# Kernel tuning notes

Hardware: AMD Instinct MI355X
Metric: run time of the kernel (lower is better)

Reference implementation:

```python
import jax, jax.numpy as jnp
import numpy as np

B, D, H1, H2, J, Q, O = 32768, 35, 256, 256, 12, 7, 5


def setup_inputs() -> dict:
    key = jax.random.key(0)
    ks = jax.random.split(key, 16)
    s = 0.05
    inp = {
        "x": jax.random.uniform(ks[0], (B, D), dtype=jnp.float32),
        "judge_ids": jax.random.randint(ks[1], (B,), 0, J, dtype=jnp.int32),
        # shared layers
        "W1_w": jax.random.normal(ks[2], (H1, D + 1), jnp.float32) * s,
        "W1_b": jnp.zeros((H1,), jnp.float32),
        "W2_w": jax.random.normal(ks[3], (H2, H1 + 1), jnp.float32) * s,
        "W2_b": jnp.zeros((H2,), jnp.float32),
        # judge-specific layers (stacked over J experts)
        "W1a_w": jax.random.normal(ks[4], (J, H1, D + 1), jnp.float32) * s,
        "W1a_b": jnp.zeros((J, H1), jnp.float32),
        "W2a_w": jax.random.normal(ks[5], (J, H2, H1 + 1), jnp.float32) * s,
        "W2a_b": jnp.zeros((J, H2), jnp.float32),
        # per-question output heads (shared + judge-specific)
        "V_w": jax.random.normal(ks[6], (Q, O, H2 + 1), jnp.float32) * s,
        "V_b": jnp.zeros((Q, O), jnp.float32),
        "Va_w": jax.random.normal(ks[7], (J, Q, O, H2 + 1), jnp.float32) * s,
        "Va_b": jnp.zeros((J, Q, O), jnp.float32),
    }
    return inp


def _append_ones(a):
    return jnp.concatenate([a, jnp.ones((a.shape[0], 1), a.dtype)], axis=1)


def reference(x, judge_ids, W1_w, W1_b, W2_w, W2_b, W1a_w, W1a_b, W2a_w, W2a_b, V_w, V_b, Va_w, Va_b):
    ids = judge_ids.astype(jnp.int32)
    xb = _append_ones(x)                                   # (B, D+1)
    # layer 1: shared + judge-routed
    a1 = jnp.einsum('bi,jhi->bjh', xb, W1a_w)              # (B, J, H1)
    j1 = jnp.take_along_axis(a1, ids[:, None, None], axis=1)[:, 0] + W1a_b[ids]
    z1 = jax.nn.relu(xb @ W1_w.T + W1_b + j1)              # (B, H1)
    z1b = _append_ones(z1)                                 # (B, H1+1)
    # layer 2
    a2 = jnp.einsum('bh,jgh->bjg', z1b, W2a_w)             # (B, J, H2)
    j2 = jnp.take_along_axis(a2, ids[:, None, None], axis=1)[:, 0] + W2a_b[ids]
    z2 = jax.nn.relu(z1b @ W2_w.T + W2_b + j2)             # (B, H2)
    z2b = _append_ones(z2)                                 # (B, H2+1)
    # per-question heads
    shared = jnp.einsum('bh,qoh->bqo', z2b, V_w) + V_b     # (B, Q, O)
    aV = jnp.einsum('bh,jqoh->bjqo', z2b, Va_w)            # (B, J, Q, O)
    jV = jnp.take_along_axis(aV, ids[:, None, None, None], axis=1)[:, 0] + Va_b[ids]
    return jax.nn.softmax(shared + jV, axis=-1)            # (B, Q, O)
```

## Files before the change

kernel.cpp:

```cpp
#include <hip/hip_runtime.h>
#include <stdint.h>

#define B_N   32768
#define D_IN  35
#define NJ    12
#define NQ    7
#define NO    5
#define QO    35
#define TILE  32
#define TPJ   128
#define CAPJ  (TPJ * TILE)
#define MAXT  1040

typedef __bf16  v8bf  __attribute__((ext_vector_type(8)));
typedef float   f32x4 __attribute__((ext_vector_type(4)));

__device__ __forceinline__ unsigned short f2bf(float f) {
    unsigned int u = __builtin_bit_cast(unsigned int, f);
    u += 0x7FFFu + ((u >> 16) & 1u);
    return (unsigned short)(u >> 16);
}
__device__ __forceinline__ unsigned int pack2(float a, float b) {
    return (unsigned int)f2bf(a) | ((unsigned int)f2bf(b) << 16);
}

__global__ void k_prep(const int* __restrict__ ids,
                       const float* __restrict__ W1_w, const float* __restrict__ W1_b,
                       const float* __restrict__ W2_w, const float* __restrict__ W2_b,
                       const float* __restrict__ W1a_w, const float* __restrict__ W1a_b,
                       const float* __restrict__ W2a_w, const float* __restrict__ W2a_b,
                       const float* __restrict__ V_w,  const float* __restrict__ V_b,
                       const float* __restrict__ Va_w, const float* __restrict__ Va_b,
                       unsigned short* __restrict__ w1c, unsigned short* __restrict__ w2c,
                       unsigned short* __restrict__ vc,
                       float* __restrict__ bias1, float* __restrict__ bias2,
                       float* __restrict__ biasv,
                       int* __restrict__ cursor, int* __restrict__ perm)
{
    const int tid = blockIdx.x * blockDim.x + threadIdx.x;
    const int nth = gridDim.x * blockDim.x;

    if (blockIdx.x < B_N / 256) {
        __shared__ int lh[NJ], lb[NJ];
        const int lt = threadIdx.x;
        const int s0 = blockIdx.x * 256;
        if (lt < NJ) lh[lt] = 0;
        __syncthreads();
        int id = ids[s0 + lt];
        int rank = atomicAdd(&lh[id], 1);
        __syncthreads();
        if (lt < NJ)
            lb[lt] = lh[lt] ? atomicAdd(&cursor[lt], lh[lt]) : 0;
        __syncthreads();
        int pos = lb[id] + rank;
        if (pos < CAPJ) perm[id * CAPJ + pos] = s0 + lt;
    }

    for (int q = tid; q < NJ * 256 * 64; q += nth) {
        int k4 = (q & 63) << 2, h = (q >> 6) & 255, jj = q >> 14;
        const float* a = &W2_w[h * 257 + k4];
        const float* b = &W2a_w[(jj * 256 + h) * 257 + k4];
        ushort4 o;
        o.x = f2bf(a[0] + b[0]); o.y = f2bf(a[1] + b[1]);
        o.z = f2bf(a[2] + b[2]); o.w = f2bf(a[3] + b[3]);
        *(ushort4*)&w2c[(size_t)q << 2] = o;
    }
    for (int q = tid; q < NJ * 256 * 16; q += nth) {
        int k4 = (q & 15) << 2, h = (q >> 4) & 255, jj = q >> 12;
        ushort4 o;
        float v[4];
#pragma unroll
        for (int e = 0; e < 4; ++e) {
            int k = k4 + e;
            v[e] = (k < D_IN) ? (W1_w[h * 36 + k] + W1a_w[(jj * 256 + h) * 36 + k]) : 0.f;
        }
        o.x = f2bf(v[0]); o.y = f2bf(v[1]); o.z = f2bf(v[2]); o.w = f2bf(v[3]);
        *(ushort4*)&w1c[(size_t)q << 2] = o;
    }
    for (int q = tid; q < NJ * 48 * 64; q += nth) {
        int k4 = (q & 63) << 2, qo = (q >> 6) % 48, jj = q / (48 * 64);
        ushort4 o;
        if (qo < QO) {
            const float* a = &V_w[qo * 257 + k4];
            const float* b = &Va_w[(jj * QO + qo) * 257 + k4];
            o.x = f2bf(a[0] + b[0]); o.y = f2bf(a[1] + b[1]);
            o.z = f2bf(a[2] + b[2]); o.w = f2bf(a[3] + b[3]);
        } else {
            o.x = o.y = o.z = o.w = 0;
        }
        *(ushort4*)&vc[(size_t)q << 2] = o;
    }
    for (int i = tid; i < NJ * 256; i += nth) {
        int h = i & 255, jj = i >> 8;
        bias1[i] = W1_w[h * 36 + 35] + W1a_w[(jj * 256 + h) * 36 + 35] + W1_b[h] + W1a_b[i];
        bias2[i] = W2_w[h * 257 + 256] + W2a_w[(jj * 256 + h) * 257 + 256] + W2_b[h] + W2a_b[i];
    }
    for (int i = tid; i < NJ * 48; i += nth) {
        int qo = i % 48, jj = i / 48;
        float v = 0.f;
        if (qo < QO) v = V_w[qo * 257 + 256] + Va_w[(jj * QO + qo) * 257 + 256]
                       + V_b[qo] + Va_b[jj * QO + qo];
        biasv[i] = v;
    }
}

__global__ __launch_bounds__(256, 4) void k_main(
    const float* __restrict__ x, float* __restrict__ out,
    const int* __restrict__ perm, const int* __restrict__ counts,
    const unsigned short* __restrict__ w1c, const unsigned short* __restrict__ w2c,
    const unsigned short* __restrict__ vc,
    const float* __restrict__ bias1, const float* __restrict__ bias2,
    const float* __restrict__ biasv)
{
    __shared__ __align__(16) unsigned short s_z1[TILE][264];
    __shared__ __align__(16) union {
        unsigned short xb[TILE][72];
        float          lg[TILE][40];
    } s_u;
    __shared__ int s_rows[TILE];

    const int bid = blockIdx.x;

    int nt = 0;
#pragma unroll
    for (int jj = 0; jj < NJ; ++jj) nt += (counts[jj] + 31) >> 5;
    if (bid >= nt) return;

    const int q8 = nt >> 3, r8 = nt & 7;
    const int xcd = bid & 7, idx = bid >> 3;
    const int lbid = (xcd < r8 ? xcd * (q8 + 1) : r8 * (q8 + 1) + (xcd - r8) * q8) + idx;

    int j = 0, tb_j = 0, cj = 0, pacc = 0;
#pragma unroll
    for (int jj = 0; jj < NJ; ++jj) {
        int c = counts[jj];
        if (lbid >= pacc) { j = jj; tb_j = pacc; cj = c; }
        pacc += (c + 31) >> 5;
    }
    if (cj > CAPJ) cj = CAPJ;
    const int ts = (lbid - tb_j) << 5;

    const int tid  = threadIdx.x;
    const int lane = tid & 63;
    const int wave = tid >> 6;
    const int l16  = lane & 15;
    const int lk   = lane >> 4;

    const unsigned short* w1p = w1c + ((size_t)j << 14) + (size_t)(wave * 64) * 64;
    v8bf w1a0[4], w1a1[4];
#pragma unroll
    for (int t = 0; t < 4; ++t) {
        const unsigned short* rp = w1p + (t * 16 + l16) * 64;
        w1a0[t] = *(const v8bf*)&rp[lk * 8];
        w1a1[t] = *(const v8bf*)&rp[32 + lk * 8];
    }

    if (tid < TILE)
        s_rows[tid] = (ts + tid < cj) ? perm[j * CAPJ + ts + tid] : -1;
    for (int i = tid; i < TILE * 36; i += 256) ((unsigned int*)s_u.xb)[i] = 0u;
    __syncthreads();

    for (int i = tid; i < TILE * D_IN; i += 256) {
        int s = i / D_IN, k = i - s * D_IN;
        int r = s_rows[s];
        s_u.xb[s][k] = f2bf(r >= 0 ? x[(size_t)r * D_IN + k] : 0.f);
    }
    __syncthreads();

    const f32x4 vz = {0.f, 0.f, 0.f, 0.f};

    {
        v8bf b1[2][2];
#pragma unroll
        for (int mt = 0; mt < 2; ++mt) {
            b1[mt][0] = *(const v8bf*)&s_u.xb[mt * 16 + l16][lk * 8];
            b1[mt][1] = *(const v8bf*)&s_u.xb[mt * 16 + l16][32 + lk * 8];
        }
        f32x4 acc[4][2];
#pragma unroll
        for (int t = 0; t < 4; ++t) { acc[t][0] = vz; acc[t][1] = vz; }
        __builtin_amdgcn_s_setprio(1);
#pragma unroll
        for (int t = 0; t < 4; ++t) {
#pragma unroll
            for (int mt = 0; mt < 2; ++mt) {
                acc[t][mt] = __builtin_amdgcn_mfma_f32_16x16x32_bf16(w1a0[t], b1[mt][0], acc[t][mt], 0, 0, 0);
                acc[t][mt] = __builtin_amdgcn_mfma_f32_16x16x32_bf16(w1a1[t], b1[mt][1], acc[t][mt], 0, 0, 0);
            }
        }
        __builtin_amdgcn_s_setprio(0);
        const unsigned short* w2p = w2c + ((size_t)j << 16) + (size_t)(wave * 64) * 256;
        v8bf a2pre[4];
#pragma unroll
        for (int gt = 0; gt < 4; ++gt)
            a2pre[gt] = *(const v8bf*)&w2p[(gt * 16 + l16) * 256 + lk * 8];

#pragma unroll
        for (int t = 0; t < 4; ++t) {
            f32x4 bz = *(const f32x4*)&bias1[j * 256 + wave * 64 + t * 16 + lk * 4];
#pragma unroll
            for (int mt = 0; mt < 2; ++mt) {
                float v0 = acc[t][mt][0] + bz[0], v1 = acc[t][mt][1] + bz[1];
                float v2 = acc[t][mt][2] + bz[2], v3 = acc[t][mt][3] + bz[3];
                v0 = v0 > 0.f ? v0 : 0.f; v1 = v1 > 0.f ? v1 : 0.f;
                v2 = v2 > 0.f ? v2 : 0.f; v3 = v3 > 0.f ? v3 : 0.f;
                uint2 pk; pk.x = pack2(v0, v1); pk.y = pack2(v2, v3);
                *(uint2*)&s_z1[mt * 16 + l16][wave * 64 + t * 16 + lk * 4] = pk;
            }
        }
        __syncthreads();

        f32x4 acc2[4][2];
#pragma unroll
        for (int gt = 0; gt < 4; ++gt) { acc2[gt][0] = vz; acc2[gt][1] = vz; }
        __builtin_amdgcn_s_setprio(1);
        {
            v8bf bb0 = *(const v8bf*)&s_z1[l16][lk * 8];
            v8bf bb1 = *(const v8bf*)&s_z1[16 + l16][lk * 8];
#pragma unroll
            for (int gt = 0; gt < 4; ++gt) {
                acc2[gt][0] = __builtin_amdgcn_mfma_f32_16x16x32_bf16(a2pre[gt], bb0, acc2[gt][0], 0, 0, 0);
                acc2[gt][1] = __builtin_amdgcn_mfma_f32_16x16x32_bf16(a2pre[gt], bb1, acc2[gt][1], 0, 0, 0);
            }
        }
#pragma unroll 2
        for (int hc = 1; hc < 8; ++hc) {
            v8bf bb0 = *(const v8bf*)&s_z1[l16][hc * 32 + lk * 8];
            v8bf bb1 = *(const v8bf*)&s_z1[16 + l16][hc * 32 + lk * 8];
#pragma unroll
            for (int gt = 0; gt < 4; ++gt) {
                v8bf a = *(const v8bf*)&w2p[(gt * 16 + l16) * 256 + hc * 32 + lk * 8];
                acc2[gt][0] = __builtin_amdgcn_mfma_f32_16x16x32_bf16(a, bb0, acc2[gt][0], 0, 0, 0);
                acc2[gt][1] = __builtin_amdgcn_mfma_f32_16x16x32_bf16(a, bb1, acc2[gt][1], 0, 0, 0);
            }
        }
        __builtin_amdgcn_s_setprio(0);
        const unsigned short* vp = vc + (size_t)j * 12288 + (size_t)(wave * 16) * 256;
        v8bf a3pre;
        if (wave < 3) a3pre = *(const v8bf*)&vp[l16 * 256 + lk * 8];

        __syncthreads();
#pragma unroll
        for (int gt = 0; gt < 4; ++gt) {
            f32x4 bz = *(const f32x4*)&bias2[j * 256 + wave * 64 + gt * 16 + lk * 4];
#pragma unroll
            for (int mt = 0; mt < 2; ++mt) {
                float v0 = acc2[gt][mt][0] + bz[0], v1 = acc2[gt][mt][1] + bz[1];
                float v2 = acc2[gt][mt][2] + bz[2], v3 = acc2[gt][mt][3] + bz[3];
                v0 = v0 > 0.f ? v0 : 0.f; v1 = v1 > 0.f ? v1 : 0.f;
                v2 = v2 > 0.f ? v2 : 0.f; v3 = v3 > 0.f ? v3 : 0.f;
                uint2 pk; pk.x = pack2(v0, v1); pk.y = pack2(v2, v3);
                *(uint2*)&s_z1[mt * 16 + l16][wave * 64 + gt * 16 + lk * 4] = pk;
            }
        }
        __syncthreads();

        if (wave < 3) {
            f32x4 av[2] = {vz, vz};
            __builtin_amdgcn_s_setprio(1);
            {
                v8bf bb0 = *(const v8bf*)&s_z1[l16][lk * 8];
                v8bf bb1 = *(const v8bf*)&s_z1[16 + l16][lk * 8];
                av[0] = __builtin_amdgcn_mfma_f32_16x16x32_bf16(a3pre, bb0, av[0], 0, 0, 0);
                av[1] = __builtin_amdgcn_mfma_f32_16x16x32_bf16(a3pre, bb1, av[1], 0, 0, 0);
            }
#pragma unroll 4
            for (int gc = 1; gc < 8; ++gc) {
                v8bf bb0 = *(const v8bf*)&s_z1[l16][gc * 32 + lk * 8];
                v8bf bb1 = *(const v8bf*)&s_z1[16 + l16][gc * 32 + lk * 8];
                v8bf a = *(const v8bf*)&vp[l16 * 256 + gc * 32 + lk * 8];
                av[0] = __builtin_amdgcn_mfma_f32_16x16x32_bf16(a, bb0, av[0], 0, 0, 0);
                av[1] = __builtin_amdgcn_mfma_f32_16x16x32_bf16(a, bb1, av[1], 0, 0, 0);
            }
            __builtin_amdgcn_s_setprio(0);
            int qb = wave * 16 + lk * 4;
            if (qb < 36) {
                f32x4 bz = *(const f32x4*)&biasv[j * 48 + qb];
#pragma unroll
                for (int mt = 0; mt < 2; ++mt) {
                    f32x4 v = av[mt] + bz;
                    *(f32x4*)&s_u.lg[mt * 16 + l16][qb] = v;
                }
            }
        }
    }
    __syncthreads();

    if (tid < TILE * NQ) {
        int s = tid / NQ, qq = tid - s * NQ;
        int r = s_rows[s];
        if (r >= 0) {
            float l[NO], mx = -1e30f;
#pragma unroll
            for (int o = 0; o < NO; ++o) {
                l[o] = s_u.lg[s][qq * NO + o];
                mx = l[o] > mx ? l[o] : mx;
            }
            float sum = 0.f, e[NO];
#pragma unroll
            for (int o = 0; o < NO; ++o) { e[o] = __expf(l[o] - mx); sum += e[o]; }
            float inv = 1.f / sum;
            float* op = out + (size_t)r * QO + qq * NO;
#pragma unroll
            for (int o = 0; o < NO; ++o) op[o] = e[o] * inv;
        }
    }
}

extern "C" void kernel_launch(void* const* d_in, const int* in_sizes, int n_in,
                              void* d_out, int out_size, void* d_ws, size_t ws_size,
                              hipStream_t stream)
{
    const float* x     = (const float*)d_in[0];
    const int*   ids   = (const int*)d_in[1];
    const float* W1_w  = (const float*)d_in[2];
    const float* W1_b  = (const float*)d_in[3];
    const float* W2_w  = (const float*)d_in[4];
    const float* W2_b  = (const float*)d_in[5];
    const float* W1a_w = (const float*)d_in[6];
    const float* W1a_b = (const float*)d_in[7];
    const float* W2a_w = (const float*)d_in[8];
    const float* W2a_b = (const float*)d_in[9];
    const float* V_w   = (const float*)d_in[10];
    const float* V_b   = (const float*)d_in[11];
    const float* Va_w  = (const float*)d_in[12];
    const float* Va_b  = (const float*)d_in[13];
    float* out = (float*)d_out;

    char* ws = (char*)d_ws;
    size_t off = 0;
    auto take = [&](size_t nbytes) -> void* {
        void* p = ws + off;
        off = (off + nbytes + 255) & ~(size_t)255;
        return p;
    };
    unsigned short* w1c = (unsigned short*)take((size_t)NJ * 256 * 64 * 2);
    unsigned short* w2c = (unsigned short*)take((size_t)NJ * 256 * 256 * 2);
    unsigned short* vc  = (unsigned short*)take((size_t)NJ * 48 * 256 * 2);
    float* bias1        = (float*)take((size_t)NJ * 256 * 4);
    float* bias2        = (float*)take((size_t)NJ * 256 * 4);
    float* biasv        = (float*)take((size_t)NJ * 48 * 4);
    int* cursor         = (int*)take(NJ * 4);
    int* perm           = (int*)take((size_t)NJ * CAPJ * 4);

    hipMemsetAsync(cursor, 0, NJ * sizeof(int), stream);
    k_prep<<<768, 256, 0, stream>>>(ids, W1_w, W1_b, W2_w, W2_b, W1a_w, W1a_b,
                                    W2a_w, W2a_b, V_w, V_b, Va_w, Va_b,
                                    w1c, w2c, vc, bias1, bias2, biasv,
                                    cursor, perm);
    k_main<<<MAXT, 256, 0, stream>>>(x, out, perm, cursor,
                                     w1c, w2c, vc, bias1, bias2, biasv);
}
```

Baseline: 47.07 us.

## Pre-sort and bf16-pack x rows per judge in prep kernel

The prep kernel now writes each input row, converted to bf16 and zero-padded to 64 columns, into a judge-sorted buffer at the same slot as its perm entry. The main kernel then loads its layer-1 MFMA operands straight from that contiguous buffer into registers, instead of gathering x through the row indices into shared memory. This removes the LDS zero-fill, the scattered gather, two block barriers and the shared union in the main kernel. In exchange the prep kernel does strided per-thread row reads and 128-byte writes, and tile tail slots read uninitialized padding that only feeds rows that are never stored.

```diff
diff --git a/kernel.cpp b/kernel.cpp
--- a/kernel.cpp
+++ b/kernel.cpp
@@ -24,7 +24,7 @@
     return (unsigned int)f2bf(a) | ((unsigned int)f2bf(b) << 16);
 }
 
-__global__ void k_prep(const int* __restrict__ ids,
+__global__ void k_prep(const int* __restrict__ ids, const float* __restrict__ x,
                        const float* __restrict__ W1_w, const float* __restrict__ W1_b,
                        const float* __restrict__ W2_w, const float* __restrict__ W2_b,
                        const float* __restrict__ W1a_w, const float* __restrict__ W1a_b,
@@ -35,7 +35,8 @@
                        unsigned short* __restrict__ vc,
                        float* __restrict__ bias1, float* __restrict__ bias2,
                        float* __restrict__ biasv,
-                       int* __restrict__ cursor, int* __restrict__ perm)
+                       int* __restrict__ cursor, int* __restrict__ perm,
+                       unsigned short* __restrict__ xsorted)
 {
     const int tid = blockIdx.x * blockDim.x + threadIdx.x;
     const int nth = gridDim.x * blockDim.x;
@@ -53,7 +54,24 @@
             lb[lt] = lh[lt] ? atomicAdd(&cursor[lt], lh[lt]) : 0;
         __syncthreads();
         int pos = lb[id] + rank;
-        if (pos < CAPJ) perm[id * CAPJ + pos] = s0 + lt;
+        if (pos < CAPJ) {
+            perm[id * CAPJ + pos] = s0 + lt;
+            const float* xr = x + (size_t)(s0 + lt) * D_IN;
+            unsigned short* xd = xsorted + ((size_t)id * CAPJ + pos) * 64;
+#pragma unroll
+            for (int c = 0; c < 8; ++c) {
+                uint4 w;
+                w.x = pack2(c * 8 + 0 < D_IN ? xr[c * 8 + 0] : 0.f,
+                            c * 8 + 1 < D_IN ? xr[c * 8 + 1] : 0.f);
+                w.y = pack2(c * 8 + 2 < D_IN ? xr[c * 8 + 2] : 0.f,
+                            c * 8 + 3 < D_IN ? xr[c * 8 + 3] : 0.f);
+                w.z = pack2(c * 8 + 4 < D_IN ? xr[c * 8 + 4] : 0.f,
+                            c * 8 + 5 < D_IN ? xr[c * 8 + 5] : 0.f);
+                w.w = pack2(c * 8 + 6 < D_IN ? xr[c * 8 + 6] : 0.f,
+                            c * 8 + 7 < D_IN ? xr[c * 8 + 7] : 0.f);
+                *(uint4*)&xd[c * 8] = w;
+            }
+        }
     }
 
     for (int q = tid; q < NJ * 256 * 64; q += nth) {
@@ -105,18 +123,16 @@
 }
 
 __global__ __launch_bounds__(256, 4) void k_main(
-    const float* __restrict__ x, float* __restrict__ out,
+    float* __restrict__ out,
     const int* __restrict__ perm, const int* __restrict__ counts,
+    const unsigned short* __restrict__ xsorted,
     const unsigned short* __restrict__ w1c, const unsigned short* __restrict__ w2c,
     const unsigned short* __restrict__ vc,
     const float* __restrict__ bias1, const float* __restrict__ bias2,
     const float* __restrict__ biasv)
 {
     __shared__ __align__(16) unsigned short s_z1[TILE][264];
-    __shared__ __align__(16) union {
-        unsigned short xb[TILE][72];
-        float          lg[TILE][40];
-    } s_u;
+    __shared__ float s_lg[TILE][40];
     __shared__ int s_rows[TILE];
 
     const int bid = blockIdx.x;
@@ -146,6 +162,17 @@
     const int l16  = lane & 15;
     const int lk   = lane >> 4;
 
+    if (tid < TILE)
+        s_rows[tid] = (ts + tid < cj) ? perm[j * CAPJ + ts + tid] : -1;
+
+    const unsigned short* xs = xsorted + ((size_t)j * CAPJ + ts) * 64;
+    v8bf b1[2][2];
+#pragma unroll
+    for (int mt = 0; mt < 2; ++mt) {
+        b1[mt][0] = *(const v8bf*)&xs[(mt * 16 + l16) * 64 + lk * 8];
+        b1[mt][1] = *(const v8bf*)&xs[(mt * 16 + l16) * 64 + 32 + lk * 8];
+    }
+
     const unsigned short* w1p = w1c + ((size_t)j << 14) + (size_t)(wave * 64) * 64;
     v8bf w1a0[4], w1a1[4];
 #pragma unroll
@@ -155,27 +182,9 @@
         w1a1[t] = *(const v8bf*)&rp[32 + lk * 8];
     }
 
-    if (tid < TILE)
-        s_rows[tid] = (ts + tid < cj) ? perm[j * CAPJ + ts + tid] : -1;
-    for (int i = tid; i < TILE * 36; i += 256) ((unsigned int*)s_u.xb)[i] = 0u;
-    __syncthreads();
-
-    for (int i = tid; i < TILE * D_IN; i += 256) {
-        int s = i / D_IN, k = i - s * D_IN;
-        int r = s_rows[s];
-        s_u.xb[s][k] = f2bf(r >= 0 ? x[(size_t)r * D_IN + k] : 0.f);
-    }
-    __syncthreads();
-
     const f32x4 vz = {0.f, 0.f, 0.f, 0.f};
 
     {
-        v8bf b1[2][2];
-#pragma unroll
-        for (int mt = 0; mt < 2; ++mt) {
-            b1[mt][0] = *(const v8bf*)&s_u.xb[mt * 16 + l16][lk * 8];
-            b1[mt][1] = *(const v8bf*)&s_u.xb[mt * 16 + l16][32 + lk * 8];
-        }
         f32x4 acc[4][2];
 #pragma unroll
         for (int t = 0; t < 4; ++t) { acc[t][0] = vz; acc[t][1] = vz; }
@@ -279,7 +288,7 @@
 #pragma unroll
                 for (int mt = 0; mt < 2; ++mt) {
                     f32x4 v = av[mt] + bz;
-                    *(f32x4*)&s_u.lg[mt * 16 + l16][qb] = v;
+                    *(f32x4*)&s_lg[mt * 16 + l16][qb] = v;
                 }
             }
         }
@@ -293,7 +302,7 @@
             float l[NO], mx = -1e30f;
 #pragma unroll
             for (int o = 0; o < NO; ++o) {
-                l[o] = s_u.lg[s][qq * NO + o];
+                l[o] = s_lg[s][qq * NO + o];
                 mx = l[o] > mx ? l[o] : mx;
             }
             float sum = 0.f, e[NO];
@@ -342,12 +351,13 @@
     float* biasv        = (float*)take((size_t)NJ * 48 * 4);
     int* cursor         = (int*)take(NJ * 4);
     int* perm           = (int*)take((size_t)NJ * CAPJ * 4);
+    unsigned short* xsorted = (unsigned short*)take((size_t)NJ * CAPJ * 64 * 2);
 
     hipMemsetAsync(cursor, 0, NJ * sizeof(int), stream);
-    k_prep<<<768, 256, 0, stream>>>(ids, W1_w, W1_b, W2_w, W2_b, W1a_w, W1a_b,
+    k_prep<<<768, 256, 0, stream>>>(ids, x, W1_w, W1_b, W2_w, W2_b, W1a_w, W1a_b,
                                     W2a_w, W2a_b, V_w, V_b, Va_w, Va_b,
                                     w1c, w2c, vc, bias1, bias2, biasv,
-                                    cursor, perm);
-    k_main<<<MAXT, 256, 0, stream>>>(x, out, perm, cursor,
+                                    cursor, perm, xsorted);
+    k_main<<<MAXT, 256, 0, stream>>>(out, perm, cursor, xsorted,
                                      w1c, w2c, vc, bias1, bias2, biasv);
 }
```

Measured after the change: 51.38 us. 1.09x slower.

## Fuse prep and main kernels into one cooperative persistent kernel with grid syncs

Applied to the files above, without the earlier changes.

Replaces the memset, prep kernel and main kernel with a single cooperative kernel. The cursor is reset in-kernel and grid-wide syncs separate the phases, and the main tile loop becomes a persistent grid-stride loop over tiles. This is meant to remove launch and inter-kernel gaps, at the cost of two grid barriers, a cooperative-launch path and possibly lower occupancy from the larger merged kernel. The host now also queries occupancy on every launch.

```diff
diff --git a/kernel.cpp b/kernel.cpp
--- a/kernel.cpp
+++ b/kernel.cpp
@@ -1,5 +1,8 @@
 #include <hip/hip_runtime.h>
+#include <hip/hip_cooperative_groups.h>
 #include <stdint.h>
+
+namespace cg = cooperative_groups;
 
 #define B_N   32768
 #define D_IN  35
@@ -10,7 +13,6 @@
 #define TILE  32
 #define TPJ   128
 #define CAPJ  (TPJ * TILE)
-#define MAXT  1040
 
 typedef __bf16  v8bf  __attribute__((ext_vector_type(8)));
 typedef float   f32x4 __attribute__((ext_vector_type(4)));
@@ -24,39 +26,52 @@
     return (unsigned int)f2bf(a) | ((unsigned int)f2bf(b) << 16);
 }
 
-__global__ void k_prep(const int* __restrict__ ids,
-                       const float* __restrict__ W1_w, const float* __restrict__ W1_b,
-                       const float* __restrict__ W2_w, const float* __restrict__ W2_b,
-                       const float* __restrict__ W1a_w, const float* __restrict__ W1a_b,
-                       const float* __restrict__ W2a_w, const float* __restrict__ W2a_b,
-                       const float* __restrict__ V_w,  const float* __restrict__ V_b,
-                       const float* __restrict__ Va_w, const float* __restrict__ Va_b,
-                       unsigned short* __restrict__ w1c, unsigned short* __restrict__ w2c,
-                       unsigned short* __restrict__ vc,
-                       float* __restrict__ bias1, float* __restrict__ bias2,
-                       float* __restrict__ biasv,
-                       int* __restrict__ cursor, int* __restrict__ perm)
+__global__ __launch_bounds__(256, 4) void k_all(
+    const float* __restrict__ x, const int* __restrict__ ids,
+    const float* __restrict__ W1_w, const float* __restrict__ W1_b,
+    const float* __restrict__ W2_w, const float* __restrict__ W2_b,
+    const float* __restrict__ W1a_w, const float* __restrict__ W1a_b,
+    const float* __restrict__ W2a_w, const float* __restrict__ W2a_b,
+    const float* __restrict__ V_w,  const float* __restrict__ V_b,
+    const float* __restrict__ Va_w, const float* __restrict__ Va_b,
+    float* __restrict__ out,
+    unsigned short* __restrict__ w1c, unsigned short* __restrict__ w2c,
+    unsigned short* __restrict__ vc,
+    float* __restrict__ bias1, float* __restrict__ bias2,
+    float* __restrict__ biasv,
+    int* __restrict__ cursor, int* __restrict__ perm)
 {
-    const int tid = blockIdx.x * blockDim.x + threadIdx.x;
-    const int nth = gridDim.x * blockDim.x;
+    __shared__ __align__(16) unsigned short s_z1[TILE][264];
+    __shared__ __align__(16) union {
+        unsigned short xb[TILE][72];
+        float          lg[TILE][40];
+    } s_u;
+    __shared__ int s_rows[TILE];
+    __shared__ int s_lh[NJ], s_lb[NJ];
+
+    cg::grid_group grid = cg::this_grid();
+    const int tid  = threadIdx.x;
+    const int gtid = blockIdx.x * blockDim.x + tid;
+    const int nth  = gridDim.x * blockDim.x;
+
+    if (blockIdx.x == 0 && tid < NJ) cursor[tid] = 0;
+    grid.sync();
 
     if (blockIdx.x < B_N / 256) {
-        __shared__ int lh[NJ], lb[NJ];
-        const int lt = threadIdx.x;
         const int s0 = blockIdx.x * 256;
-        if (lt < NJ) lh[lt] = 0;
-        __syncthreads();
-        int id = ids[s0 + lt];
-        int rank = atomicAdd(&lh[id], 1);
-        __syncthreads();
-        if (lt < NJ)
-            lb[lt] = lh[lt] ? atomicAdd(&cursor[lt], lh[lt]) : 0;
-        __syncthreads();
-        int pos = lb[id] + rank;
-        if (pos < CAPJ) perm[id * CAPJ + pos] = s0 + lt;
-    }
-
-    for (int q = tid; q < NJ * 256 * 64; q += nth) {
+        if (tid < NJ) s_lh[tid] = 0;
+        __syncthreads();
+        int id = ids[s0 + tid];
+        int rank = atomicAdd(&s_lh[id], 1);
+        __syncthreads();
+        if (tid < NJ)
+            s_lb[tid] = s_lh[tid] ? atomicAdd(&cursor[tid], s_lh[tid]) : 0;
+        __syncthreads();
+        int pos = s_lb[id] + rank;
+        if (pos < CAPJ) perm[id * CAPJ + pos] = s0 + tid;
+    }
+
+    for (int q = gtid; q < NJ * 256 * 64; q += nth) {
         int k4 = (q & 63) << 2, h = (q >> 6) & 255, jj = q >> 14;
         const float* a = &W2_w[h * 257 + k4];
         const float* b = &W2a_w[(jj * 256 + h) * 257 + k4];
@@ -65,7 +80,7 @@
         o.z = f2bf(a[2] + b[2]); o.w = f2bf(a[3] + b[3]);
         *(ushort4*)&w2c[(size_t)q << 2] = o;
     }
-    for (int q = tid; q < NJ * 256 * 16; q += nth) {
+    for (int q = gtid; q < NJ * 256 * 16; q += nth) {
         int k4 = (q & 15) << 2, h = (q >> 4) & 255, jj = q >> 12;
         ushort4 o;
         float v[4];
@@ -77,7 +92,7 @@
         o.x = f2bf(v[0]); o.y = f2bf(v[1]); o.z = f2bf(v[2]); o.w = f2bf(v[3]);
         *(ushort4*)&w1c[(size_t)q << 2] = o;
     }
-    for (int q = tid; q < NJ * 48 * 64; q += nth) {
+    for (int q = gtid; q < NJ * 48 * 64; q += nth) {
         int k4 = (q & 63) << 2, qo = (q >> 6) % 48, jj = q / (48 * 64);
         ushort4 o;
         if (qo < QO) {
@@ -90,220 +105,208 @@
         }
         *(ushort4*)&vc[(size_t)q << 2] = o;
     }
-    for (int i = tid; i < NJ * 256; i += nth) {
+    for (int i = gtid; i < NJ * 256; i += nth) {
         int h = i & 255, jj = i >> 8;
         bias1[i] = W1_w[h * 36 + 35] + W1a_w[(jj * 256 + h) * 36 + 35] + W1_b[h] + W1a_b[i];
         bias2[i] = W2_w[h * 257 + 256] + W2a_w[(jj * 256 + h) * 257 + 256] + W2_b[h] + W2a_b[i];
     }
-    for (int i = tid; i < NJ * 48; i += nth) {
+    for (int i = gtid; i < NJ * 48; i += nth) {
         int qo = i % 48, jj = i / 48;
         float v = 0.f;
         if (qo < QO) v = V_w[qo * 257 + 256] + Va_w[(jj * QO + qo) * 257 + 256]
                        + V_b[qo] + Va_b[jj * QO + qo];
         biasv[i] = v;
     }
-}
-
-__global__ __launch_bounds__(256, 4) void k_main(
-    const float* __restrict__ x, float* __restrict__ out,
-    const int* __restrict__ perm, const int* __restrict__ counts,
-    const unsigned short* __restrict__ w1c, const unsigned short* __restrict__ w2c,
-    const unsigned short* __restrict__ vc,
-    const float* __restrict__ bias1, const float* __restrict__ bias2,
-    const float* __restrict__ biasv)
-{
-    __shared__ __align__(16) unsigned short s_z1[TILE][264];
-    __shared__ __align__(16) union {
-        unsigned short xb[TILE][72];
-        float          lg[TILE][40];
-    } s_u;
-    __shared__ int s_rows[TILE];
-
-    const int bid = blockIdx.x;
-
-    int nt = 0;
-#pragma unroll
-    for (int jj = 0; jj < NJ; ++jj) nt += (counts[jj] + 31) >> 5;
-    if (bid >= nt) return;
-
-    const int q8 = nt >> 3, r8 = nt & 7;
-    const int xcd = bid & 7, idx = bid >> 3;
-    const int lbid = (xcd < r8 ? xcd * (q8 + 1) : r8 * (q8 + 1) + (xcd - r8) * q8) + idx;
-
-    int j = 0, tb_j = 0, cj = 0, pacc = 0;
+    grid.sync();
+
+    int c0, nt = 0;
+    int cnt_[NJ];
 #pragma unroll
     for (int jj = 0; jj < NJ; ++jj) {
-        int c = counts[jj];
-        if (lbid >= pacc) { j = jj; tb_j = pacc; cj = c; }
-        pacc += (c + 31) >> 5;
-    }
-    if (cj > CAPJ) cj = CAPJ;
-    const int ts = (lbid - tb_j) << 5;
-
-    const int tid  = threadIdx.x;
+        c0 = cursor[jj];
+        cnt_[jj] = c0;
+        nt += (c0 + 31) >> 5;
+    }
+
     const int lane = tid & 63;
     const int wave = tid >> 6;
     const int l16  = lane & 15;
     const int lk   = lane >> 4;
-
-    const unsigned short* w1p = w1c + ((size_t)j << 14) + (size_t)(wave * 64) * 64;
-    v8bf w1a0[4], w1a1[4];
-#pragma unroll
-    for (int t = 0; t < 4; ++t) {
-        const unsigned short* rp = w1p + (t * 16 + l16) * 64;
-        w1a0[t] = *(const v8bf*)&rp[lk * 8];
-        w1a1[t] = *(const v8bf*)&rp[32 + lk * 8];
-    }
-
-    if (tid < TILE)
-        s_rows[tid] = (ts + tid < cj) ? perm[j * CAPJ + ts + tid] : -1;
-    for (int i = tid; i < TILE * 36; i += 256) ((unsigned int*)s_u.xb)[i] = 0u;
-    __syncthreads();
-
-    for (int i = tid; i < TILE * D_IN; i += 256) {
-        int s = i / D_IN, k = i - s * D_IN;
-        int r = s_rows[s];
-        s_u.xb[s][k] = f2bf(r >= 0 ? x[(size_t)r * D_IN + k] : 0.f);
-    }
-    __syncthreads();
-
     const f32x4 vz = {0.f, 0.f, 0.f, 0.f};
 
-    {
-        v8bf b1[2][2];
-#pragma unroll
-        for (int mt = 0; mt < 2; ++mt) {
-            b1[mt][0] = *(const v8bf*)&s_u.xb[mt * 16 + l16][lk * 8];
-            b1[mt][1] = *(const v8bf*)&s_u.xb[mt * 16 + l16][32 + lk * 8];
-        }
-        f32x4 acc[4][2];
-#pragma unroll
-        for (int t = 0; t < 4; ++t) { acc[t][0] = vz; acc[t][1] = vz; }
-        __builtin_amdgcn_s_setprio(1);
+    for (int bid = blockIdx.x; bid < nt; bid += gridDim.x) {
+        const int q8 = nt >> 3, r8 = nt & 7;
+        const int xcd = bid & 7, idx = bid >> 3;
+        const int lbid = (xcd < r8 ? xcd * (q8 + 1) : r8 * (q8 + 1) + (xcd - r8) * q8) + idx;
+
+        int j = 0, tb_j = 0, cj = 0, pacc = 0;
+#pragma unroll
+        for (int jj = 0; jj < NJ; ++jj) {
+            int c = cnt_[jj];
+            if (lbid >= pacc) { j = jj; tb_j = pacc; cj = c; }
+            pacc += (c + 31) >> 5;
+        }
+        if (cj > CAPJ) cj = CAPJ;
+        const int ts = (lbid - tb_j) << 5;
+
+        const unsigned short* w1p = w1c + ((size_t)j << 14) + (size_t)(wave * 64) * 64;
+        v8bf w1a0[4], w1a1[4];
 #pragma unroll
         for (int t = 0; t < 4; ++t) {
+            const unsigned short* rp = w1p + (t * 16 + l16) * 64;
+            w1a0[t] = *(const v8bf*)&rp[lk * 8];
+            w1a1[t] = *(const v8bf*)&rp[32 + lk * 8];
+        }
+
+        if (tid < TILE)
+            s_rows[tid] = (ts + tid < cj) ? perm[j * CAPJ + ts + tid] : -1;
+        for (int i = tid; i < TILE * 36; i += 256) ((unsigned int*)s_u.xb)[i] = 0u;
+        __syncthreads();
+
+        for (int i = tid; i < TILE * D_IN; i += 256) {
+            int s = i / D_IN, k = i - s * D_IN;
+            int r = s_rows[s];
+            s_u.xb[s][k] = f2bf(r >= 0 ? x[(size_t)r * D_IN + k] : 0.f);
+        }
+        __syncthreads();
+
+        {
+            v8bf b1[2][2];
 #pragma unroll
             for (int mt = 0; mt < 2; ++mt) {
-                acc[t][mt] = __builtin_amdgcn_mfma_f32_16x16x32_bf16(w1a0[t], b1[mt][0], acc[t][mt], 0, 0, 0);
-                acc[t][mt] = __builtin_amdgcn_mfma_f32_16x16x32_bf16(w1a1[t], b1[mt][1], acc[t][mt], 0, 0, 0);
-            }
-        }
-        __builtin_amdgcn_s_setprio(0);
-        const unsigned short* w2p = w2c + ((size_t)j << 16) + (size_t)(wave * 64) * 256;
-        v8bf a2pre[4];
-#pragma unroll
-        for (int gt = 0; gt < 4; ++gt)
-            a2pre[gt] = *(const v8bf*)&w2p[(gt * 16 + l16) * 256 + lk * 8];
-
-#pragma unroll
-        for (int t = 0; t < 4; ++t) {
-            f32x4 bz = *(const f32x4*)&bias1[j * 256 + wave * 64 + t * 16 + lk * 4];
-#pragma unroll
-            for (int mt = 0; mt < 2; ++mt) {
-                float v0 = acc[t][mt][0] + bz[0], v1 = acc[t][mt][1] + bz[1];
-                float v2 = acc[t][mt][2] + bz[2], v3 = acc[t][mt][3] + bz[3];
-                v0 = v0 > 0.f ? v0 : 0.f; v1 = v1 > 0.f ? v1 : 0.f;
-                v2 = v2 > 0.f ? v2 : 0.f; v3 = v3 > 0.f ? v3 : 0.f;
-                uint2 pk; pk.x = pack2(v0, v1); pk.y = pack2(v2, v3);
-                *(uint2*)&s_z1[mt * 16 + l16][wave * 64 + t * 16 + lk * 4] = pk;
-            }
-        }
-        __syncthreads();
-
-        f32x4 acc2[4][2];
-#pragma unroll
-        for (int gt = 0; gt < 4; ++gt) { acc2[gt][0] = vz; acc2[gt][1] = vz; }
-        __builtin_amdgcn_s_setprio(1);
-        {
-            v8bf bb0 = *(const v8bf*)&s_z1[l16][lk * 8];
-            v8bf bb1 = *(const v8bf*)&s_z1[16 + l16][lk * 8];
-#pragma unroll
-            for (int gt = 0; gt < 4; ++gt) {
-                acc2[gt][0] = __builtin_amdgcn_mfma_f32_16x16x32_bf16(a2pre[gt], bb0, acc2[gt][0], 0, 0, 0);
-                acc2[gt][1] = __builtin_amdgcn_mfma_f32_16x16x32_bf16(a2pre[gt], bb1, acc2[gt][1], 0, 0, 0);
-            }
-        }
-#pragma unroll 2
-        for (int hc = 1; hc < 8; ++hc) {
-            v8bf bb0 = *(const v8bf*)&s_z1[l16][hc * 32 + lk * 8];
-            v8bf bb1 = *(const v8bf*)&s_z1[16 + l16][hc * 32 + lk * 8];
-#pragma unroll
-            for (int gt = 0; gt < 4; ++gt) {
-                v8bf a = *(const v8bf*)&w2p[(gt * 16 + l16) * 256 + hc * 32 + lk * 8];
-                acc2[gt][0] = __builtin_amdgcn_mfma_f32_16x16x32_bf16(a, bb0, acc2[gt][0], 0, 0, 0);
-                acc2[gt][1] = __builtin_amdgcn_mfma_f32_16x16x32_bf16(a, bb1, acc2[gt][1], 0, 0, 0);
-            }
-        }
-        __builtin_amdgcn_s_setprio(0);
-        const unsigned short* vp = vc + (size_t)j * 12288 + (size_t)(wave * 16) * 256;
-        v8bf a3pre;
-        if (wave < 3) a3pre = *(const v8bf*)&vp[l16 * 256 + lk * 8];
-
-        __syncthreads();
-#pragma unroll
-        for (int gt = 0; gt < 4; ++gt) {
-            f32x4 bz = *(const f32x4*)&bias2[j * 256 + wave * 64 + gt * 16 + lk * 4];
-#pragma unroll
-            for (int mt = 0; mt < 2; ++mt) {
-                float v0 = acc2[gt][mt][0] + bz[0], v1 = acc2[gt][mt][1] + bz[1];
-                float v2 = acc2[gt][mt][2] + bz[2], v3 = acc2[gt][mt][3] + bz[3];
-                v0 = v0 > 0.f ? v0 : 0.f; v1 = v1 > 0.f ? v1 : 0.f;
-                v2 = v2 > 0.f ? v2 : 0.f; v3 = v3 > 0.f ? v3 : 0.f;
-                uint2 pk; pk.x = pack2(v0, v1); pk.y = pack2(v2, v3);
-                *(uint2*)&s_z1[mt * 16 + l16][wave * 64 + gt * 16 + lk * 4] = pk;
-            }
-        }
-        __syncthreads();
-
-        if (wave < 3) {
-            f32x4 av[2] = {vz, vz};
+                b1[mt][0] = *(const v8bf*)&s_u.xb[mt * 16 + l16][lk * 8];
+                b1[mt][1] = *(const v8bf*)&s_u.xb[mt * 16 + l16][32 + lk * 8];
+            }
+            f32x4 acc[4][2];
+#pragma unroll
+            for (int t = 0; t < 4; ++t) { acc[t][0] = vz; acc[t][1] = vz; }
+            __builtin_amdgcn_s_setprio(1);
+#pragma unroll
+            for (int t = 0; t < 4; ++t) {
+#pragma unroll
+                for (int mt = 0; mt < 2; ++mt) {
+                    acc[t][mt] = __builtin_amdgcn_mfma_f32_16x16x32_bf16(w1a0[t], b1[mt][0], acc[t][mt], 0, 0, 0);
+                    acc[t][mt] = __builtin_amdgcn_mfma_f32_16x16x32_bf16(w1a1[t], b1[mt][1], acc[t][mt], 0, 0, 0);
+                }
+            }
+            __builtin_amdgcn_s_setprio(0);
+            const unsigned short* w2p = w2c + ((size_t)j << 16) + (size_t)(wave * 64) * 256;
+            v8bf a2pre[4];
+#pragma unroll
+            for (int gt = 0; gt < 4; ++gt)
+                a2pre[gt] = *(const v8bf*)&w2p[(gt * 16 + l16) * 256 + lk * 8];
+
+#pragma unroll
+            for (int t = 0; t < 4; ++t) {
+                f32x4 bz = *(const f32x4*)&bias1[j * 256 + wave * 64 + t * 16 + lk * 4];
+#pragma unroll
+                for (int mt = 0; mt < 2; ++mt) {
+                    float v0 = acc[t][mt][0] + bz[0], v1 = acc[t][mt][1] + bz[1];
+                    float v2 = acc[t][mt][2] + bz[2], v3 = acc[t][mt][3] + bz[3];
+                    v0 = v0 > 0.f ? v0 : 0.f; v1 = v1 > 0.f ? v1 : 0.f;
+                    v2 = v2 > 0.f ? v2 : 0.f; v3 = v3 > 0.f ? v3 : 0.f;
+                    uint2 pk; pk.x = pack2(v0, v1); pk.y = pack2(v2, v3);
+                    *(uint2*)&s_z1[mt * 16 + l16][wave * 64 + t * 16 + lk * 4] = pk;
+                }
+            }
+            __syncthreads();
+
+            f32x4 acc2[4][2];
+#pragma unroll
+            for (int gt = 0; gt < 4; ++gt) { acc2[gt][0] = vz; acc2[gt][1] = vz; }
             __builtin_amdgcn_s_setprio(1);
             {
                 v8bf bb0 = *(const v8bf*)&s_z1[l16][lk * 8];
                 v8bf bb1 = *(const v8bf*)&s_z1[16 + l16][lk * 8];
-                av[0] = __builtin_amdgcn_mfma_f32_16x16x32_bf16(a3pre, bb0, av[0], 0, 0, 0);
-                av[1] = __builtin_amdgcn_mfma_f32_16x16x32_bf16(a3pre, bb1, av[1], 0, 0, 0);
-            }
+#pragma unroll
+                for (int gt = 0; gt < 4; ++gt) {
+                    acc2[gt][0] = __builtin_amdgcn_mfma_f32_16x16x32_bf16(a2pre[gt], bb0, acc2[gt][0], 0, 0, 0);
+                    acc2[gt][1] = __builtin_amdgcn_mfma_f32_16x16x32_bf16(a2pre[gt], bb1, acc2[gt][1], 0, 0, 0);
+                }
+            }
+#pragma unroll 2
+            for (int hc = 1; hc < 8; ++hc) {
+                v8bf bb0 = *(const v8bf*)&s_z1[l16][hc * 32 + lk * 8];
+                v8bf bb1 = *(const v8bf*)&s_z1[16 + l16][hc * 32 + lk * 8];
+#pragma unroll
+                for (int gt = 0; gt < 4; ++gt) {
+                    v8bf a = *(const v8bf*)&w2p[(gt * 16 + l16) * 256 + hc * 32 + lk * 8];
+                    acc2[gt][0] = __builtin_amdgcn_mfma_f32_16x16x32_bf16(a, bb0, acc2[gt][0], 0, 0, 0);
+                    acc2[gt][1] = __builtin_amdgcn_mfma_f32_16x16x32_bf16(a, bb1, acc2[gt][1], 0, 0, 0);
+                }
+            }
+            __builtin_amdgcn_s_setprio(0);
+            const unsigned short* vp = vc + (size_t)j * 12288 + (size_t)(wave * 16) * 256;
+            v8bf a3pre;
+            if (wave < 3) a3pre = *(const v8bf*)&vp[l16 * 256 + lk * 8];
+
+            __syncthreads();
+#pragma unroll
+            for (int gt = 0; gt < 4; ++gt) {
+                f32x4 bz = *(const f32x4*)&bias2[j * 256 + wave * 64 + gt * 16 + lk * 4];
+#pragma unroll
+                for (int mt = 0; mt < 2; ++mt) {
+                    float v0 = acc2[gt][mt][0] + bz[0], v1 = acc2[gt][mt][1] + bz[1];
+                    float v2 = acc2[gt][mt][2] + bz[2], v3 = acc2[gt][mt][3] + bz[3];
+                    v0 = v0 > 0.f ? v0 : 0.f; v1 = v1 > 0.f ? v1 : 0.f;
+                    v2 = v2 > 0.f ? v2 : 0.f; v3 = v3 > 0.f ? v3 : 0.f;
+                    uint2 pk; pk.x = pack2(v0, v1); pk.y = pack2(v2, v3);
+                    *(uint2*)&s_z1[mt * 16 + l16][wave * 64 + gt * 16 + lk * 4] = pk;
+                }
+            }
+            __syncthreads();
+
+            if (wave < 3) {
+                f32x4 av[2] = {vz, vz};
+                __builtin_amdgcn_s_setprio(1);
+                {
+                    v8bf bb0 = *(const v8bf*)&s_z1[l16][lk * 8];
+                    v8bf bb1 = *(const v8bf*)&s_z1[16 + l16][lk * 8];
+                    av[0] = __builtin_amdgcn_mfma_f32_16x16x32_bf16(a3pre, bb0, av[0], 0, 0, 0);
+                    av[1] = __builtin_amdgcn_mfma_f32_16x16x32_bf16(a3pre, bb1, av[1], 0, 0, 0);
+                }
 #pragma unroll 4
-            for (int gc = 1; gc < 8; ++gc) {
-                v8bf bb0 = *(const v8bf*)&s_z1[l16][gc * 32 + lk * 8];
-                v8bf bb1 = *(const v8bf*)&s_z1[16 + l16][gc * 32 + lk * 8];
-                v8bf a = *(const v8bf*)&vp[l16 * 256 + gc * 32 + lk * 8];
-                av[0] = __builtin_amdgcn_mfma_f32_16x16x32_bf16(a, bb0, av[0], 0, 0, 0);
-                av[1] = __builtin_amdgcn_mfma_f32_16x16x32_bf16(a, bb1, av[1], 0, 0, 0);
-            }
-            __builtin_amdgcn_s_setprio(0);
-            int qb = wave * 16 + lk * 4;
-            if (qb < 36) {
-                f32x4 bz = *(const f32x4*)&biasv[j * 48 + qb];
-#pragma unroll
-                for (int mt = 0; mt < 2; ++mt) {
-                    f32x4 v = av[mt] + bz;
-                    *(f32x4*)&s_u.lg[mt * 16 + l16][qb] = v;
-                }
-            }
-        }
-    }
-    __syncthreads();
-
-    if (tid < TILE * NQ) {
-        int s = tid / NQ, qq = tid - s * NQ;
-        int r = s_rows[s];
-        if (r >= 0) {
-            float l[NO], mx = -1e30f;
-#pragma unroll
-            for (int o = 0; o < NO; ++o) {
-                l[o] = s_u.lg[s][qq * NO + o];
-                mx = l[o] > mx ? l[o] : mx;
-            }
-            float sum = 0.f, e[NO];
-#pragma unroll
-            for (int o = 0; o < NO; ++o) { e[o] = __expf(l[o] - mx); sum += e[o]; }
-            float inv = 1.f / sum;
-            float* op = out + (size_t)r * QO + qq * NO;
-#pragma unroll
-            for (int o = 0; o < NO; ++o) op[o] = e[o] * inv;
-        }
+                for (int gc = 1; gc < 8; ++gc) {
+                    v8bf bb0 = *(const v8bf*)&s_z1[l16][gc * 32 + lk * 8];
+                    v8bf bb1 = *(const v8bf*)&s_z1[16 + l16][gc * 32 + lk * 8];
+                    v8bf a = *(const v8bf*)&vp[l16 * 256 + gc * 32 + lk * 8];
+                    av[0] = __builtin_amdgcn_mfma_f32_16x16x32_bf16(a, bb0, av[0], 0, 0, 0);
+                    av[1] = __builtin_amdgcn_mfma_f32_16x16x32_bf16(a, bb1, av[1], 0, 0, 0);
+                }
+                __builtin_amdgcn_s_setprio(0);
+                int qb = wave * 16 + lk * 4;
+                if (qb < 36) {
+                    f32x4 bz = *(const f32x4*)&biasv[j * 48 + qb];
+#pragma unroll
+                    for (int mt = 0; mt < 2; ++mt) {
+                        f32x4 v = av[mt] + bz;
+                        *(f32x4*)&s_u.lg[mt * 16 + l16][qb] = v;
+                    }
+                }
+            }
+        }
+        __syncthreads();
+
+        if (tid < TILE * NQ) {
+            int s = tid / NQ, qq = tid - s * NQ;
+            int r = s_rows[s];
+            if (r >= 0) {
+                float l[NO], mx = -1e30f;
+#pragma unroll
+                for (int o = 0; o < NO; ++o) {
+                    l[o] = s_u.lg[s][qq * NO + o];
+                    mx = l[o] > mx ? l[o] : mx;
+                }
+                float sum = 0.f, e[NO];
+#pragma unroll
+                for (int o = 0; o < NO; ++o) { e[o] = __expf(l[o] - mx); sum += e[o]; }
+                float inv = 1.f / sum;
+                float* op = out + (size_t)r * QO + qq * NO;
+#pragma unroll
+                for (int o = 0; o < NO; ++o) op[o] = e[o] * inv;
+            }
+        }
+        __syncthreads();
     }
 }
 
@@ -343,11 +346,21 @@
     int* cursor         = (int*)take(NJ * 4);
     int* perm           = (int*)take((size_t)NJ * CAPJ * 4);
 
-    hipMemsetAsync(cursor, 0, NJ * sizeof(int), stream);
-    k_prep<<<768, 256, 0, stream>>>(ids, W1_w, W1_b, W2_w, W2_b, W1a_w, W1a_b,
-                                    W2a_w, W2a_b, V_w, V_b, Va_w, Va_b,
-                                    w1c, w2c, vc, bias1, bias2, biasv,
-                                    cursor, perm);
-    k_main<<<MAXT, 256, 0, stream>>>(x, out, perm, cursor,
-                                     w1c, w2c, vc, bias1, bias2, biasv);
+    int maxPerCU = 0;
+    hipOccupancyMaxActiveBlocksPerMultiprocessor(&maxPerCU, k_all, 256, 0);
+    int grid = (maxPerCU > 0 ? maxPerCU : 4) * 256;
+    if (grid > 1024) grid = 1024;
+    if (grid < 128)  grid = 128;
+
+    void* args[] = {
+        (void*)&x, (void*)&ids,
+        (void*)&W1_w, (void*)&W1_b, (void*)&W2_w, (void*)&W2_b,
+        (void*)&W1a_w, (void*)&W1a_b, (void*)&W2a_w, (void*)&W2a_b,
+        (void*)&V_w, (void*)&V_b, (void*)&Va_w, (void*)&Va_b,
+        (void*)&out,
+        (void*)&w1c, (void*)&w2c, (void*)&vc,
+        (void*)&bias1, (void*)&bias2, (void*)&biasv,
+        (void*)&cursor, (void*)&perm
+    };
+    hipLaunchCooperativeKernel((void*)k_all, dim3(grid), dim3(256), args, 0, stream);
 }
```

Result: slower. 153.2 us (+225.5%).
